# Optimization experiments

Hardware: AMD Instinct MI355X
Metric: run time of the kernel (lower is better)

## Reference

```python
import jax, jax.numpy as jnp
import numpy as np

VOCAB = 50001
EMBED = 64
HIDDEN = 100
OUT = 1


def setup_inputs() -> dict:
    key = jax.random.key(0)
    ks = jax.random.split(key, 8)
    B, T = 2048, 512
    x = jax.random.randint(ks[0], (B, T), 0, VOCAB, dtype=jnp.int64)
    s_e = 1.0  # nn.Embedding default N(0,1)
    s_r = 1.0 / np.sqrt(HIDDEN)  # nn.RNN / nn.Linear uniform(-1/sqrt(fan), 1/sqrt(fan))
    embed_table = jax.random.normal(ks[1], (VOCAB, EMBED), dtype=jnp.float32) * s_e
    W_ih = jax.random.uniform(ks[2], (HIDDEN, EMBED), jnp.float32, -s_r, s_r)
    W_hh = jax.random.uniform(ks[3], (HIDDEN, HIDDEN), jnp.float32, -s_r, s_r)
    b_ih = jax.random.uniform(ks[4], (HIDDEN,), jnp.float32, -s_r, s_r)
    b_hh = jax.random.uniform(ks[5], (HIDDEN,), jnp.float32, -s_r, s_r)
    fc_W = jax.random.uniform(ks[6], (OUT, HIDDEN), jnp.float32, -s_r, s_r)
    fc_b = jax.random.uniform(ks[7], (OUT,), jnp.float32, -s_r, s_r)
    return {"x": x, "embed_table": embed_table, "W_ih": W_ih, "W_hh": W_hh,
            "b_ih": b_ih, "b_hh": b_hh, "fc_W": fc_W, "fc_b": fc_b}


def reference(x, embed_table, W_ih, W_hh, b_ih, b_hh, fc_W, fc_b):
    B = x.shape[0]
    embeds = embed_table[x]                       # [B, T, E]
    # Precompute input projection for all timesteps in one GEMM.
    xproj = jnp.einsum('bte,he->bth', embeds, W_ih) + b_ih + b_hh  # [B, T, H]
    h0 = jnp.zeros((B, HIDDEN), dtype=embeds.dtype)

    def step(h, xp_t):
        h_new = jnp.tanh(xp_t + h @ W_hh.T)       # [B, H]
        return h_new, None

    h_final, _ = jax.lax.scan(step, h0, jnp.swapaxes(xproj, 0, 1))  # scan over T
    logits = h_final @ fc_W.T + fc_b              # [B, 1]
    return jax.nn.sigmoid(logits)
```

## Files before the change

kernel.cpp:

```cpp
#include <hip/hip_runtime.h>
#include <hip/hip_bf16.h>
#include <cstdint>

#define VOCAB  50001
#define EMBED  64
#define HIDDEN 100
#define TSTEPS 512
#define BATCH  2048

typedef short bf16x8 __attribute__((ext_vector_type(8)));
typedef float f32x4  __attribute__((ext_vector_type(4)));

constexpr int RB = 16;
constexpr int KP = 128;
constexpr int UP = 128;
constexpr int NBLK = BATCH / RB;

constexpr size_t WHH_BYTES = (size_t)UP * KP * 2;
constexpr size_t P_OFF     = 2 * WHH_BYTES;
constexpr size_t P_BYTES   = (size_t)VOCAB * HIDDEN * 4;
constexpr size_t WS_NEED   = P_OFF + P_BYTES;

__device__ __forceinline__ float fast_tanh(float x) {
  const float e = __expf(2.0f * x);
  return 1.0f - 2.0f * __builtin_amdgcn_rcpf(e + 1.0f);
}
__device__ __forceinline__ unsigned cvt_pk_bf16(float a, float b) {
  unsigned r;
  asm("v_cvt_pk_bf16_f32 %0, %1, %2" : "=v"(r) : "v"(a), "v"(b));
  return r;
}
__device__ __forceinline__ f32x4 zf4() { f32x4 z = {0.f, 0.f, 0.f, 0.f}; return z; }

#define MFMA16(A,B,C) __builtin_amdgcn_mfma_f32_16x16x32_bf16((A),(B),(C),0,0,0)

__global__ __launch_bounds__(128) void proj_kernel(
    const float* __restrict__ table, const float* __restrict__ Wih,
    const float* __restrict__ bih, const float* __restrict__ bhh,
    float* __restrict__ P)
{
  constexpr int VPB = 16;
  __shared__ float e[VPB][EMBED];
  const int vbase = blockIdx.x * VPB;
  const int tid = threadIdx.x;
  #pragma unroll
  for (int r = 0; r < VPB * EMBED / 128; ++r) {
    const int el = tid + 128 * r;
    const int v  = vbase + (el >> 6);
    e[el >> 6][el & 63] = (v < VOCAB) ? table[(size_t)v * EMBED + (el & 63)] : 0.f;
  }
  __syncthreads();

  const int j = (tid < HIDDEN) ? tid : HIDDEN - 1;
  float w[EMBED];
  #pragma unroll
  for (int k = 0; k < EMBED; k += 4) {
    const float4 t4 = *reinterpret_cast<const float4*>(&Wih[j * EMBED + k]);
    w[k] = t4.x; w[k+1] = t4.y; w[k+2] = t4.z; w[k+3] = t4.w;
  }
  const float bias = bih[j] + bhh[j];

  for (int r = 0; r < VPB; ++r) {
    const int v = vbase + r;
    if (v >= VOCAB) break;
    float acc = bias;
    #pragma unroll
    for (int k = 0; k < EMBED; k += 4) {
      const float4 ev = *reinterpret_cast<const float4*>(&e[r][k]);
      acc += w[k]*ev.x + w[k+1]*ev.y + w[k+2]*ev.z + w[k+3]*ev.w;
    }
    if (tid < HIDDEN) P[(size_t)v * HIDDEN + tid] = acc;
  }
}

__global__ __launch_bounds__(256) void prep_whh(
    const float* __restrict__ Whh, unsigned short* __restrict__ hi,
    unsigned short* __restrict__ lo)
{
  const int i = blockIdx.x * 256 + threadIdx.x;
  if (i >= UP * KP) return;
  const int u = i >> 7, k = i & (KP - 1);
  const float v = (u < HIDDEN && k < HIDDEN) ? Whh[u * HIDDEN + k] : 0.f;
  const unsigned b = __float_as_uint(v);
  const unsigned h16 = (b + 0x7FFFu + ((b >> 16) & 1u)) >> 16;
  const float hf = __uint_as_float(h16 << 16);
  const float r = v - hf;
  const unsigned rb = __float_as_uint(r);
  const unsigned l16 = (rb + 0x7FFFu + ((rb >> 16) & 1u)) >> 16;
  hi[i] = (unsigned short)h16;
  lo[i] = (unsigned short)l16;
}

__global__ __launch_bounds__(512, 1)
void rnn_mfma_kernel(const int* __restrict__ x, const unsigned char* __restrict__ ws,
                     const float* __restrict__ fcW, const float* __restrict__ fcb,
                     float* __restrict__ out)
{
  __shared__ __align__(16) unsigned char hbuf[2][4096];
  __shared__ int idx_lds[TSTEPS][RB];
  __shared__ float red[64];

  const int tid = threadIdx.x;
  const int w   = tid >> 6;
  const int l   = tid & 63;
  const int row = l & 15;
  const int g   = l >> 4;
  const int row0 = blockIdx.x * RB;
  const unsigned swz = (unsigned)((row & 7) << 4);

  reinterpret_cast<uint4*>(&hbuf[0][0])[tid] = make_uint4(0u, 0u, 0u, 0u);

  {
    const int r = tid >> 5, tl = tid & 31;
    const int* __restrict__ xr = x + (size_t)(row0 + r) * TSTEPS;
    #pragma unroll
    for (int c = 0; c < TSTEPS / 32; ++c) {
      const int t = tl + 32 * c;
      idx_lds[t][r] = xr[t];
    }
  }

  const unsigned char* __restrict__ WH = ws;
  const unsigned char* __restrict__ WL = ws + WHH_BYTES;
  const float* __restrict__ Pb = reinterpret_cast<const float*>(ws + P_OFF);

  bf16x8 whi[4], wlo[4];
  #pragma unroll
  for (int kt = 0; kt < 4; ++kt) {
    const unsigned off = (unsigned)(w * 16 + row) * 256u + (unsigned)(kt * 64 + g * 16);
    whi[kt] = *reinterpret_cast<const bf16x8*>(WH + off);
    wlo[kt] = *reinterpret_cast<const bf16x8*>(WL + off);
  }

  const int useed  = w * 16 + g * 4;
  const int useedc = (useed <= 96) ? useed : 96;

  __syncthreads();

  f32x4 SA, SB;
  {
    const int x0 = idx_lds[0][row];
    const int x1 = idx_lds[1][row];
    SA = *reinterpret_cast<const f32x4*>(Pb + (size_t)x0 * HIDDEN + useedc);
    SB = *reinterpret_cast<const f32x4*>(Pb + (size_t)x1 * HIDDEN + useedc);
  }

  auto body = [&](int t, const unsigned char* hbR, unsigned char* hbW, f32x4 &S) {
    bf16x8 bhi[4];
    #pragma unroll
    for (int kt = 0; kt < 4; ++kt) {
      const unsigned off = ((unsigned)(row * 256 + kt * 64 + g * 16)) ^ swz;
      bhi[kt] = *reinterpret_cast<const bf16x8*>(hbR + off);
    }
    f32x4 a1 = S, a3 = zf4();
    #pragma unroll
    for (int kt = 0; kt < 4; ++kt) {
      a1 = MFMA16(whi[kt], bhi[kt], a1);
      a3 = MFMA16(wlo[kt], bhi[kt], a3);
    }
    const f32x4 d0 = a1 + a3;
    {
      const int tn = (t + 2 < TSTEPS) ? t + 2 : TSTEPS - 1;
      const int xt = idx_lds[tn][row];
      S = *reinterpret_cast<const f32x4*>(Pb + (size_t)xt * HIDDEN + useedc);
    }
    {
      const unsigned ph01 = cvt_pk_bf16(fast_tanh(d0[0]), fast_tanh(d0[1]));
      const unsigned ph23 = cvt_pk_bf16(fast_tanh(d0[2]), fast_tanh(d0[3]));
      const unsigned off = ((unsigned)(row * 256 + useed * 2)) ^ swz;
      *reinterpret_cast<uint2*>(hbW + off) = make_uint2(ph01, ph23);
    }
    __syncthreads();
  };

  for (int t = 0; t < TSTEPS; t += 2) {
    body(t,     &hbuf[0][0], &hbuf[1][0], SA);
    body(t + 1, &hbuf[1][0], &hbuf[0][0], SB);
  }

  if (w == 0) {
    const unsigned char* hbF = &hbuf[0][0];
    float part = 0.f;
    for (int i = 0; i < 25; ++i) {
      const int u = g * 25 + i;
      const unsigned off = ((unsigned)(row * 256 + u * 2)) ^ swz;
      const unsigned short vh = *reinterpret_cast<const unsigned short*>(hbF + off);
      const float hv = __uint_as_float((unsigned)vh << 16);
      part += hv * fcW[u];
    }
    red[l] = part;
  }
  __syncthreads();
  if (tid < RB) {
    const float s = red[tid] + red[tid + 16] + red[tid + 32] + red[tid + 48] + fcb[0];
    out[row0 + tid] = 1.0f / (1.0f + __expf(-s));
  }
}

__global__ __launch_bounds__(64)
__attribute__((amdgpu_waves_per_eu(2, 2)))
void rnn_wave_kernel(
    const int* __restrict__ x, const float* __restrict__ P,
    const float* __restrict__ Whh,
    const float* __restrict__ fcW, const float* __restrict__ fcb,
    float* __restrict__ out)
{
  __shared__ float h_lds[2][112];
  const int row = blockIdx.x;
  const int l = threadIdx.x;
  const int u0 = l;
  const bool m1 = (l < HIDDEN - 64);
  const int u1 = m1 ? (64 + l) : (HIDDEN - 1);

  float w0[HIDDEN], w1[HIDDEN];
  #pragma unroll
  for (int k = 0; k < HIDDEN; k += 4) {
    const float4 a = *reinterpret_cast<const float4*>(&Whh[u0 * HIDDEN + k]);
    w0[k] = a.x; w0[k+1] = a.y; w0[k+2] = a.z; w0[k+3] = a.w;
    const float4 b = *reinterpret_cast<const float4*>(&Whh[u1 * HIDDEN + k]);
    w1[k] = b.x; w1[k+1] = b.y; w1[k+2] = b.z; w1[k+3] = b.w;
  }
  const float fw0 = fcW[u0];
  const float fw1 = m1 ? fcW[u1] : 0.f;

  h_lds[0][l] = 0.f;
  h_lds[0][l + 48] = 0.f;

  const int* __restrict__ xrow = x + (size_t)row * TSTEPS;
  const int i0 = xrow[0];
  float xp0 = P[i0 * HIDDEN + u0];
  float xp1 = P[i0 * HIDDEN + u1];
  int i_nx = xrow[1];

  float h0 = 0.f, h1 = 0.f;
  for (int t = 0; t < TSTEPS; ++t) {
    const int cur = t & 1, nxt = cur ^ 1;
    const float* __restrict__ Prow = P + i_nx * HIDDEN;
    const float xp0n = Prow[u0];
    const float xp1n = Prow[u1];
    i_nx = (t + 2 < TSTEPS) ? xrow[t + 2] : 0;

    float a0 = xp0, b0 = 0.f, a1v = xp1, b1 = 0.f;
    const float4* __restrict__ hb = reinterpret_cast<const float4*>(&h_lds[cur][0]);
    #pragma unroll
    for (int gq = 0; gq < HIDDEN / 4; ++gq) {
      const float4 hv = hb[gq];
      const int k = 4 * gq;
      if ((gq & 1) == 0) {
        a0  += w0[k]*hv.x + w0[k+1]*hv.y + w0[k+2]*hv.z + w0[k+3]*hv.w;
        a1v += w1[k]*hv.x + w1[k+1]*hv.y + w1[k+2]*hv.z + w1[k+3]*hv.w;
      } else {
        b0 += w0[k]*hv.x + w0[k+1]*hv.y + w0[k+2]*hv.z + w0[k+3]*hv.w;
        b1 += w1[k]*hv.x + w1[k+1]*hv.y + w1[k+2]*hv.z + w1[k+3]*hv.w;
      }
    }
    h0 = fast_tanh(a0 + b0);
    h1 = fast_tanh(a1v + b1);
    h_lds[nxt][u0] = h0;
    if (m1) h_lds[nxt][u1] = h1;
    xp0 = xp0n; xp1 = xp1n;
  }

  float s = h0 * fw0 + (m1 ? h1 * fw1 : 0.f);
  #pragma unroll
  for (int off = 32; off > 0; off >>= 1) s += __shfl_down(s, off);
  if (l == 0) out[row] = 1.0f / (1.0f + __expf(-(s + fcb[0])));
}

extern "C" void kernel_launch(void* const* d_in, const int* in_sizes, int n_in,
                              void* d_out, int out_size, void* d_ws, size_t ws_size,
                              hipStream_t stream) {
  const int*   x     = (const int*)  d_in[0];
  const float* table = (const float*)d_in[1];
  const float* Wih   = (const float*)d_in[2];
  const float* Whh   = (const float*)d_in[3];
  const float* bih   = (const float*)d_in[4];
  const float* bhh   = (const float*)d_in[5];
  const float* fcW   = (const float*)d_in[6];
  const float* fcb   = (const float*)d_in[7];
  float* out = (float*)d_out;

  unsigned char* ws = (unsigned char*)d_ws;

  if (ws_size >= WS_NEED) {
    unsigned short* WhhHi = (unsigned short*)ws;
    unsigned short* WhhLo = (unsigned short*)(ws + WHH_BYTES);
    float* Pt = (float*)(ws + P_OFF);
    prep_whh<<<(UP * KP + 255) / 256, 256, 0, stream>>>(Whh, WhhHi, WhhLo);
    proj_kernel<<<(VOCAB + 15) / 16, 128, 0, stream>>>(table, Wih, bih, bhh, Pt);
    rnn_mfma_kernel<<<NBLK, 512, 0, stream>>>(x, ws, fcW, fcb, out);
  } else {
    float* Pt = (float*)ws;
    proj_kernel<<<(VOCAB + 15) / 16, 128, 0, stream>>>(table, Wih, bih, bhh, Pt);
    rnn_wave_kernel<<<BATCH, 64, 0, stream>>>(x, Pt, Whh, fcW, fcb, out);
  }
}
```

Measured before the change: 280.3 us.

## Drop bf16 low-residual MFMAs and handle K tail with scalar FP32

Removes the lo-part W_hh MFMAs and the padded fourth K-tile in the recurrent step. K 0..95 now uses three hi-only bf16 MFMAs split across two accumulators, and the last four hidden inputs use FP32 weights loaded into registers. The padding-only wave skips compute and only joins the barrier. This shortens the per-step dependent MFMA chain in the serial recurrence, at the cost of reduced W_hh precision, which may affect accuracy.

```diff
diff --git a/kernel.cpp b/kernel.cpp
--- a/kernel.cpp
+++ b/kernel.cpp
@@ -93,6 +93,7 @@
 
 __global__ __launch_bounds__(512, 1)
 void rnn_mfma_kernel(const int* __restrict__ x, const unsigned char* __restrict__ ws,
+                     const float* __restrict__ Whh,
                      const float* __restrict__ fcW, const float* __restrict__ fcb,
                      float* __restrict__ out)
 {
@@ -121,54 +122,74 @@
   }
 
   const unsigned char* __restrict__ WH = ws;
-  const unsigned char* __restrict__ WL = ws + WHH_BYTES;
   const float* __restrict__ Pb = reinterpret_cast<const float*>(ws + P_OFF);
 
-  bf16x8 whi[4], wlo[4];
-  #pragma unroll
-  for (int kt = 0; kt < 4; ++kt) {
+  bf16x8 whi[3];
+  #pragma unroll
+  for (int kt = 0; kt < 3; ++kt) {
     const unsigned off = (unsigned)(w * 16 + row) * 256u + (unsigned)(kt * 64 + g * 16);
     whi[kt] = *reinterpret_cast<const bf16x8*>(WH + off);
-    wlo[kt] = *reinterpret_cast<const bf16x8*>(WL + off);
-  }
-
-  const int useed  = w * 16 + g * 4;
-  const int useedc = (useed <= 96) ? useed : 96;
+  }
+
+  const int  useed  = w * 16 + g * 4;
+  const bool alive  = (useed <= 96);
+  const int  useedc = alive ? useed : 96;
+
+  float4 wt[4];
+  if (alive) {
+    #pragma unroll
+    for (int j = 0; j < 4; ++j)
+      wt[j] = *reinterpret_cast<const float4*>(&Whh[(useed + j) * HIDDEN + 96]);
+  } else {
+    wt[0] = wt[1] = wt[2] = wt[3] = make_float4(0.f, 0.f, 0.f, 0.f);
+  }
 
   __syncthreads();
 
   f32x4 SA, SB;
   {
-    const int x0 = idx_lds[0][row];
-    const int x1 = idx_lds[1][row];
+    const int x0 = alive ? idx_lds[0][row] : 0;
+    const int x1 = alive ? idx_lds[1][row] : 0;
     SA = *reinterpret_cast<const f32x4*>(Pb + (size_t)x0 * HIDDEN + useedc);
     SB = *reinterpret_cast<const f32x4*>(Pb + (size_t)x1 * HIDDEN + useedc);
   }
 
   auto body = [&](int t, const unsigned char* hbR, unsigned char* hbW, f32x4 &S) {
-    bf16x8 bhi[4];
-    #pragma unroll
-    for (int kt = 0; kt < 4; ++kt) {
-      const unsigned off = ((unsigned)(row * 256 + kt * 64 + g * 16)) ^ swz;
-      bhi[kt] = *reinterpret_cast<const bf16x8*>(hbR + off);
-    }
-    f32x4 a1 = S, a3 = zf4();
-    #pragma unroll
-    for (int kt = 0; kt < 4; ++kt) {
-      a1 = MFMA16(whi[kt], bhi[kt], a1);
-      a3 = MFMA16(wlo[kt], bhi[kt], a3);
-    }
-    const f32x4 d0 = a1 + a3;
-    {
-      const int tn = (t + 2 < TSTEPS) ? t + 2 : TSTEPS - 1;
-      const int xt = idx_lds[tn][row];
-      S = *reinterpret_cast<const f32x4*>(Pb + (size_t)xt * HIDDEN + useedc);
-    }
-    {
-      const unsigned ph01 = cvt_pk_bf16(fast_tanh(d0[0]), fast_tanh(d0[1]));
-      const unsigned ph23 = cvt_pk_bf16(fast_tanh(d0[2]), fast_tanh(d0[3]));
-      const unsigned off = ((unsigned)(row * 256 + useed * 2)) ^ swz;
-      *reinterpret_cast<uint2*>(hbW + off) = make_uint2(ph01, ph23);
+    if (w < 7) {
+      bf16x8 bhi[3];
+      #pragma unroll
+      for (int kt = 0; kt < 3; ++kt) {
+        const unsigned off = ((unsigned)(row * 256 + kt * 64 + g * 16)) ^ swz;
+        bhi[kt] = *reinterpret_cast<const bf16x8*>(hbR + off);
+      }
+      const unsigned tailoff = ((unsigned)(row * 256 + 192)) ^ swz;
+      const uint2 q = *reinterpret_cast<const uint2*>(hbR + tailoff);
+
+      f32x4 a = MFMA16(whi[0], bhi[0], S);
+      f32x4 b = MFMA16(whi[1], bhi[1], zf4());
+      a = MFMA16(whi[2], bhi[2], a);
+
+      const float f0 = __uint_as_float(q.x << 16);
+      const float f1 = __uint_as_float(q.x & 0xFFFF0000u);
+      const float f2 = __uint_as_float(q.y << 16);
+      const float f3 = __uint_as_float(q.y & 0xFFFF0000u);
+
+      f32x4 d;
+      #pragma unroll
+      for (int j = 0; j < 4; ++j)
+        d[j] = (a[j] + b[j]) + (wt[j].x*f0 + wt[j].y*f1 + wt[j].z*f2 + wt[j].w*f3);
+
+      {
+        const int tn = (t + 2 < TSTEPS) ? t + 2 : TSTEPS - 1;
+        const int xt = alive ? idx_lds[tn][row] : 0;
+        S = *reinterpret_cast<const f32x4*>(Pb + (size_t)xt * HIDDEN + useedc);
+      }
+      if (alive) {
+        const unsigned ph01 = cvt_pk_bf16(fast_tanh(d[0]), fast_tanh(d[1]));
+        const unsigned ph23 = cvt_pk_bf16(fast_tanh(d[2]), fast_tanh(d[3]));
+        const unsigned off = ((unsigned)(row * 256 + useed * 2)) ^ swz;
+        *reinterpret_cast<uint2*>(hbW + off) = make_uint2(ph01, ph23);
+      }
     }
     __syncthreads();
   };
@@ -288,7 +309,7 @@
     float* Pt = (float*)(ws + P_OFF);
     prep_whh<<<(UP * KP + 255) / 256, 256, 0, stream>>>(Whh, WhhHi, WhhLo);
     proj_kernel<<<(VOCAB + 15) / 16, 128, 0, stream>>>(table, Wih, bih, bhh, Pt);
-    rnn_mfma_kernel<<<NBLK, 512, 0, stream>>>(x, ws, fcW, fcb, out);
+    rnn_mfma_kernel<<<NBLK, 512, 0, stream>>>(x, ws, Whh, fcW, fcb, out);
   } else {
     float* Pt = (float*)ws;
     proj_kernel<<<(VOCAB + 15) / 16, 128, 0, stream>>>(table, Wih, bih, bhh, Pt);
```

Measured after the change: 314.5 us. +12.2%, slower.

## Process two independent 16-row batch groups per block to interleave recurrence chains

Applied to the files above, without the earlier changes.

Doubles the batch rows per workgroup from 16 to 32 and processes them as two independent recurrence streams, each with its own double-buffered hidden state. MFMAs, gathers and tanh for the two groups are interleaved so one group's work can hide the other's latency, and the two groups share one barrier per step. This halves the number of blocks (64 instead of 128), which may leave CUs idle on a large GPU. Token indices are also stored as 16-bit in LDS so the index table still fits.

```diff
diff --git a/kernel.cpp b/kernel.cpp
--- a/kernel.cpp
+++ b/kernel.cpp
@@ -11,7 +11,7 @@
 typedef short bf16x8 __attribute__((ext_vector_type(8)));
 typedef float f32x4  __attribute__((ext_vector_type(4)));
 
-constexpr int RB = 16;
+constexpr int RB = 32;
 constexpr int KP = 128;
 constexpr int UP = 128;
 constexpr int NBLK = BATCH / RB;
@@ -96,9 +96,10 @@
                      const float* __restrict__ fcW, const float* __restrict__ fcb,
                      float* __restrict__ out)
 {
-  __shared__ __align__(16) unsigned char hbuf[2][4096];
-  __shared__ int idx_lds[TSTEPS][RB];
-  __shared__ float red[64];
+  __shared__ __align__(16) unsigned char hbufA[2][4096];
+  __shared__ __align__(16) unsigned char hbufB[2][4096];
+  __shared__ unsigned short idx_lds[TSTEPS][RB];
+  __shared__ float red[2][64];
 
   const int tid = threadIdx.x;
   const int w   = tid >> 6;
@@ -108,15 +109,16 @@
   const int row0 = blockIdx.x * RB;
   const unsigned swz = (unsigned)((row & 7) << 4);
 
-  reinterpret_cast<uint4*>(&hbuf[0][0])[tid] = make_uint4(0u, 0u, 0u, 0u);
+  reinterpret_cast<uint4*>(&hbufA[0][0])[tid] = make_uint4(0u, 0u, 0u, 0u);
+  reinterpret_cast<uint4*>(&hbufB[0][0])[tid] = make_uint4(0u, 0u, 0u, 0u);
 
   {
-    const int r = tid >> 5, tl = tid & 31;
+    const int r = tid >> 4, tl = tid & 15;
     const int* __restrict__ xr = x + (size_t)(row0 + r) * TSTEPS;
     #pragma unroll
-    for (int c = 0; c < TSTEPS / 32; ++c) {
-      const int t = tl + 32 * c;
-      idx_lds[t][r] = xr[t];
+    for (int c = 0; c < TSTEPS / 16; ++c) {
+      const int t = tl + 16 * c;
+      idx_lds[t][r] = (unsigned short)xr[t];
     }
   }
 
@@ -137,49 +139,62 @@
 
   __syncthreads();
 
-  f32x4 SA, SB;
+  f32x4 SAe, SAo, SBe, SBo;
   {
-    const int x0 = idx_lds[0][row];
-    const int x1 = idx_lds[1][row];
-    SA = *reinterpret_cast<const f32x4*>(Pb + (size_t)x0 * HIDDEN + useedc);
-    SB = *reinterpret_cast<const f32x4*>(Pb + (size_t)x1 * HIDDEN + useedc);
-  }
-
-  auto body = [&](int t, const unsigned char* hbR, unsigned char* hbW, f32x4 &S) {
-    bf16x8 bhi[4];
+    const int a0 = idx_lds[0][row],      a1 = idx_lds[1][row];
+    const int b0 = idx_lds[0][16 + row], b1 = idx_lds[1][16 + row];
+    SAe = *reinterpret_cast<const f32x4*>(Pb + (size_t)a0 * HIDDEN + useedc);
+    SAo = *reinterpret_cast<const f32x4*>(Pb + (size_t)a1 * HIDDEN + useedc);
+    SBe = *reinterpret_cast<const f32x4*>(Pb + (size_t)b0 * HIDDEN + useedc);
+    SBo = *reinterpret_cast<const f32x4*>(Pb + (size_t)b1 * HIDDEN + useedc);
+  }
+
+  auto fused = [&](int t, const unsigned char* rA, unsigned char* wA,
+                   const unsigned char* rB, unsigned char* wB,
+                   f32x4 &Sa, f32x4 &Sb) {
+    bf16x8 bA[4], bB[4];
     #pragma unroll
     for (int kt = 0; kt < 4; ++kt) {
       const unsigned off = ((unsigned)(row * 256 + kt * 64 + g * 16)) ^ swz;
-      bhi[kt] = *reinterpret_cast<const bf16x8*>(hbR + off);
-    }
-    f32x4 a1 = S, a3 = zf4();
+      bA[kt] = *reinterpret_cast<const bf16x8*>(rA + off);
+      bB[kt] = *reinterpret_cast<const bf16x8*>(rB + off);
+    }
+    f32x4 a1 = Sa, a3 = zf4(), b1 = Sb, b3 = zf4();
     #pragma unroll
     for (int kt = 0; kt < 4; ++kt) {
-      a1 = MFMA16(whi[kt], bhi[kt], a1);
-      a3 = MFMA16(wlo[kt], bhi[kt], a3);
-    }
-    const f32x4 d0 = a1 + a3;
+      a1 = MFMA16(whi[kt], bA[kt], a1);
+      b1 = MFMA16(whi[kt], bB[kt], b1);
+      a3 = MFMA16(wlo[kt], bA[kt], a3);
+      b3 = MFMA16(wlo[kt], bB[kt], b3);
+    }
+    const f32x4 dA = a1 + a3;
+    const f32x4 dB = b1 + b3;
     {
       const int tn = (t + 2 < TSTEPS) ? t + 2 : TSTEPS - 1;
-      const int xt = idx_lds[tn][row];
-      S = *reinterpret_cast<const f32x4*>(Pb + (size_t)xt * HIDDEN + useedc);
+      const int xa = idx_lds[tn][row];
+      const int xb = idx_lds[tn][16 + row];
+      Sa = *reinterpret_cast<const f32x4*>(Pb + (size_t)xa * HIDDEN + useedc);
+      Sb = *reinterpret_cast<const f32x4*>(Pb + (size_t)xb * HIDDEN + useedc);
     }
     {
-      const unsigned ph01 = cvt_pk_bf16(fast_tanh(d0[0]), fast_tanh(d0[1]));
-      const unsigned ph23 = cvt_pk_bf16(fast_tanh(d0[2]), fast_tanh(d0[3]));
+      const unsigned pa01 = cvt_pk_bf16(fast_tanh(dA[0]), fast_tanh(dA[1]));
+      const unsigned pa23 = cvt_pk_bf16(fast_tanh(dA[2]), fast_tanh(dA[3]));
+      const unsigned pb01 = cvt_pk_bf16(fast_tanh(dB[0]), fast_tanh(dB[1]));
+      const unsigned pb23 = cvt_pk_bf16(fast_tanh(dB[2]), fast_tanh(dB[3]));
       const unsigned off = ((unsigned)(row * 256 + useed * 2)) ^ swz;
-      *reinterpret_cast<uint2*>(hbW + off) = make_uint2(ph01, ph23);
+      *reinterpret_cast<uint2*>(wA + off) = make_uint2(pa01, pa23);
+      *reinterpret_cast<uint2*>(wB + off) = make_uint2(pb01, pb23);
     }
     __syncthreads();
   };
 
   for (int t = 0; t < TSTEPS; t += 2) {
-    body(t,     &hbuf[0][0], &hbuf[1][0], SA);
-    body(t + 1, &hbuf[1][0], &hbuf[0][0], SB);
-  }
-
-  if (w == 0) {
-    const unsigned char* hbF = &hbuf[0][0];
+    fused(t,     &hbufA[0][0], &hbufA[1][0], &hbufB[0][0], &hbufB[1][0], SAe, SBe);
+    fused(t + 1, &hbufA[1][0], &hbufA[0][0], &hbufB[1][0], &hbufB[0][0], SAo, SBo);
+  }
+
+  if (w < 2) {
+    const unsigned char* hbF = (w == 0) ? &hbufA[0][0] : &hbufB[0][0];
     float part = 0.f;
     for (int i = 0; i < 25; ++i) {
       const int u = g * 25 + i;
@@ -188,12 +203,14 @@
       const float hv = __uint_as_float((unsigned)vh << 16);
       part += hv * fcW[u];
     }
-    red[l] = part;
+    red[w][l] = part;
   }
   __syncthreads();
   if (tid < RB) {
-    const float s = red[tid] + red[tid + 16] + red[tid + 32] + red[tid + 48] + fcb[0];
-    out[row0 + tid] = 1.0f / (1.0f + __expf(-s));
+    const int grp = tid >> 4, r = tid & 15;
+    const float s = red[grp][r] + red[grp][r + 16] + red[grp][r + 32] +
+                    red[grp][r + 48] + fcb[0];
+    out[row0 + grp * 16 + r] = 1.0f / (1.0f + __expf(-s));
   }
 }
 
```

New measurement: 415.1 us. 1.48x slower.
